# Kernel tuning notes

Hardware: AMD Instinct MI355X
Metric: run time of the kernel (lower is better)

Reference implementation:

```python
import jax, jax.numpy as jnp
import numpy as np
from math import factorial

P = 3          # polynomial order
D_I = 4096     # sketch output dim per order
C = 512        # input channels
B, H, W = 8, 28, 28
GAMMA = 1e-4


def setup_inputs() -> dict:
    key = jax.random.key(0)
    k1, k2, k3 = jax.random.split(key, 3)
    x = jax.random.normal(k1, (B, H, W, C), dtype=jnp.float32)
    # AlphaInitializer: alpha_i = sqrt(exp(-2g) * (2g)^i / i!)
    gam2 = np.full(P + 1, 2.0 * GAMMA)
    numer = np.power(gam2, np.arange(P + 1))
    denom = np.array([factorial(i) for i in range(P + 1)], dtype=np.float64)
    alpha = jnp.asarray(np.sqrt(np.exp(-gam2) * numer / denom), dtype=jnp.float32)
    # count-sketch hash indices and sign bits, one pair per order t in [0, p)
    h_idx = jax.random.randint(k2, (P, C), 0, D_I)
    s_bits = jax.random.randint(k3, (P, C), 0, 2).astype(jnp.int32)
    return {"x": x, "alpha": alpha, "h_idx": h_idx, "s_bits": s_bits}


def reference(x, alpha, h_idx, s_bits):
    Bs, Hs, Ws, Ch = x.shape
    p = h_idx.shape[0]
    d_i = D_I
    signs = (2 * s_bits - 1).astype(x.dtype)          # (p, C) in {-1,+1}
    x_flat = x.reshape(-1, Ch)                        # (B*H*W, C)

    def count_sketch(h, s):
        # scatter-add channels into d_i buckets: equivalent to x_flat @ S
        return jnp.zeros((x_flat.shape[0], d_i), x.dtype).at[:, h].add(x_flat * s)

    sk = jax.vmap(count_sketch)(h_idx, signs)         # (p, N, d_i)
    xs = jnp.transpose(sk, (1, 0, 2)).reshape(Bs, Hs * Ws, p, d_i)

    xf = jnp.fft.fft(xs.astype(jnp.complex64), axis=-1)
    cp = jnp.cumprod(xf, axis=-2)[:, :, 1:, :]        # orders 2..p
    xi = jnp.real(jnp.fft.ifft(cp, axis=-1)).mean(axis=1)   # (B, p-1, d_i)

    x_p = xi * alpha[2:].reshape(1, p - 1, 1)
    zeroth = alpha[0] * jnp.ones((Bs, 1), x.dtype)
    first = alpha[1] * x.mean(axis=(1, 2))            # (B, C)
    phi = jnp.concatenate([zeroth, first, x_p.reshape(Bs, -1)], axis=-1)
    phi = jnp.sign(phi) * jnp.sqrt(jnp.abs(phi) + 1e-12)    # signed sqrt
    return phi / jnp.linalg.norm(phi, axis=-1, keepdims=True)
```

## Files before the change

### kernel.cpp

```cpp
#include <hip/hip_runtime.h>

#define BATCH 8
#define NPOS 784
#define CH 512
#define DI 4096
#define PPC 8
#define CHUNKS (NPOS / PPC)
#define PHI_LEN 8705
#define REP 16
#define S_STRIDE (BATCH * 2 * 2049 * 2)
#define S_FLOATS (REP * S_STRIDE)
#define FO_OFF S_FLOATS
#define FO_STRIDE (BATCH * CH)
#define FO_FLOATS (REP * FO_STRIDE)
#define PH_OFF (FO_OFF + FO_FLOATS)
#define ZERO_FLOATS (S_FLOATS + FO_FLOATS)

__device__ __forceinline__ float2 cmul(float2 a, float2 b) {
  return make_float2(a.x * b.x - a.y * b.y, a.x * b.y + a.y * b.x);
}
__device__ __forceinline__ float2 f2add(float2 a, float2 b) {
  return make_float2(a.x + b.x, a.y + b.y);
}
__device__ __forceinline__ float2 f2sub(float2 a, float2 b) {
  return make_float2(a.x - b.x, a.y - b.y);
}

__device__ __forceinline__ void dft4(float2& a, float2& b, float2& c, float2& d) {
  float t0x = a.x + c.x, t0y = a.y + c.y;
  float t1x = a.x - c.x, t1y = a.y - c.y;
  float t2x = b.x + d.x, t2y = b.y + d.y;
  float t3x = b.x - d.x, t3y = b.y - d.y;
  a = make_float2(t0x + t2x, t0y + t2y);
  c = make_float2(t0x - t2x, t0y - t2y);
  b = make_float2(t1x + t3y, t1y - t3x);
  d = make_float2(t1x - t3y, t1y + t3x);
}

__device__ __forceinline__ void dft8(float2 v[8]) {
  float2 e0 = v[0], e1 = v[2], e2 = v[4], e3 = v[6];
  dft4(e0, e1, e2, e3);
  float2 o0 = v[1], o1 = v[3], o2 = v[5], o3 = v[7];
  dft4(o0, o1, o2, o3);
  const float r = 0.70710678118654752f;
  o1 = make_float2(r * (o1.x + o1.y), r * (o1.y - o1.x));
  o2 = make_float2(o2.y, -o2.x);
  o3 = make_float2(r * (o3.y - o3.x), -r * (o3.x + o3.y));
  v[0] = f2add(e0, o0); v[4] = f2sub(e0, o0);
  v[1] = f2add(e1, o1); v[5] = f2sub(e1, o1);
  v[2] = f2add(e2, o2); v[6] = f2sub(e2, o2);
  v[3] = f2add(e3, o3); v[7] = f2sub(e3, o3);
}

__device__ __forceinline__ void twiddle8(float2 v[8], float2 w) {
  float2 w2 = cmul(w, w);
  float2 w3 = cmul(w2, w);
  float2 w4 = cmul(w2, w2);
  v[1] = cmul(v[1], w);
  v[2] = cmul(v[2], w2);
  v[3] = cmul(v[3], w3);
  v[4] = cmul(v[4], w4);
  v[5] = cmul(v[5], cmul(w4, w));
  v[6] = cmul(v[6], cmul(w4, w2));
  v[7] = cmul(v[7], cmul(w4, w3));
}

__device__ __forceinline__ void s0w(float2* Z, int b) {
  const int base = b << 3;
  const int m0 = (b >> 1) & 15;
  float2 v[8];
  #pragma unroll
  for (int u = 0; u < 8; ++u) v[u] = Z[(base + u) ^ m0];
  dft8(v);
  #pragma unroll
  for (int k = 0; k < 8; ++k) Z[(base + k) ^ m0] = v[k];
}
__device__ __forceinline__ void s1w(float2* Z, int b, float2 w) {
  const int base = ((b >> 3) << 6) + (b & 7);
  const int g4 = (b >> 3) << 2;
  float2 v[8];
  #pragma unroll
  for (int u = 0; u < 8; ++u)
    v[u] = Z[(base + (u << 3)) ^ ((g4 + (u >> 1)) & 15)];
  twiddle8(v, w);
  dft8(v);
  #pragma unroll
  for (int k = 0; k < 8; ++k)
    Z[(base + (k << 3)) ^ ((g4 + (k >> 1)) & 15)] = v[k];
}
__device__ __forceinline__ void s2w(float2* Z, int b, float2 w) {
  const int base = ((b >> 6) << 9) + (b & 63);
  const int jh = (b & 63) >> 4;
  float2 v[8];
  #pragma unroll
  for (int u = 0; u < 8; ++u)
    v[u] = Z[(base + (u << 6)) ^ (((u << 2) + jh) & 15)];
  twiddle8(v, w);
  dft8(v);
  #pragma unroll
  for (int k = 0; k < 8; ++k)
    Z[(base + (k << 6)) ^ (((k << 2) + jh) & 15)] = v[k];
}
__device__ __forceinline__ void s3w(float2* Z, int b, float2 w) {
  const int m3 = (b >> 4) & 15;
  float2 v[8];
  #pragma unroll
  for (int u = 0; u < 8; ++u) v[u] = Z[(b + (u << 9)) ^ m3];
  twiddle8(v, w);
  dft8(v);
  #pragma unroll
  for (int k = 0; k < 8; ++k) Z[(b + (k << 9)) ^ m3] = v[k];
}

template <int MODE>
__device__ __forceinline__ void prodpair(float2 Zk, float2 Zm, float2& carry,
                                         float2& acc2, float2& acc3) {
  float2 E = make_float2(0.5f * (Zk.x + Zm.x), 0.5f * (Zk.y - Zm.y));
  float2 O = make_float2(0.5f * (Zk.y + Zm.y), -0.5f * (Zk.x - Zm.x));
  if (MODE == 0) {
    float2 P = cmul(E, O);
    carry = P;
    acc2.x += P.x; acc2.y += P.y;
  } else if (MODE == 1) {
    float2 P3 = cmul(carry, E);
    acc3.x += P3.x; acc3.y += P3.y;
    carry = O;
  } else {
    float2 P = cmul(carry, E);
    acc2.x += P.x; acc2.y += P.y;
    float2 P3 = cmul(P, O);
    acc3.x += P3.x; acc3.y += P3.y;
  }
}
template <int MODE>
__device__ __forceinline__ void nyq(float2 Zq, float& carryx, float& acc2x,
                                    float& acc3x) {
  if (MODE == 0) { carryx = Zq.x * Zq.y; acc2x += carryx; }
  else if (MODE == 1) { acc3x += carryx * Zq.x; carryx = Zq.y; }
  else { float tt = carryx * Zq.x; acc2x += tt; acc3x += tt * Zq.y; }
}

template <int MODE>
__device__ __forceinline__ void product_phase(float2* Z, int t,
                                              float2 carry[8], float2 acc2[8],
                                              float2 acc3[8], float& carryx,
                                              float& acc2x, float& acc3x) {
  const int mask3 = (t >> 4) & 15;
  #pragma unroll
  for (int jj = 0; jj < 8; ++jj) {
    const int k = t + (jj << 8);
    const int ak = k ^ mask3;
    const int m = (DI - k) & (DI - 1);
    const int am = m ^ ((m >> 4) & 15);
    float2 Zk = Z[ak], Zm = Z[am];
    Z[ak] = make_float2(0.f, 0.f);
    Z[am] = make_float2(0.f, 0.f);
    prodpair<MODE>(Zk, Zm, carry[jj], acc2[jj], acc3[jj]);
  }
  if (t == 0) {
    float2 Zq = Z[2048];
    Z[2048] = make_float2(0.f, 0.f);
    nyq<MODE>(Zq, carryx, acc2x, acc3x);
  }
}

__global__ __launch_bounds__(256) void cbp_stage1(
    const float* __restrict__ x, const float* __restrict__ alpha,
    const int* __restrict__ h_idx, const int* __restrict__ s_bits,
    float* __restrict__ ws) {
  __shared__ float2 Z[DI];
  float* Zf = (float*)Z;
  const int t = threadIdx.x;
  const int bb = blockIdx.x / CHUNKS;
  const int ch = blockIdx.x % CHUNKS;
  const int rep = blockIdx.x & (REP - 1);

  auto mapq = [](int h, int s) {
    int r = ((h & 7) << 9) | (((h >> 3) & 7) << 6) | (((h >> 6) & 7) << 3) |
            (h >> 9);
    return (r ^ ((r >> 4) & 15)) | ((s ^ 1) << 12);
  };
  auto sgn = [](float v, int q) {
    return __int_as_float(__float_as_int(v) ^ ((q & 0x1000) << 19));
  };
  const int c0 = t * 2, c1 = c0 + 1;
  const int qp0 = mapq(h_idx[c0], s_bits[c0]) |
                  (mapq(h_idx[c1], s_bits[c1]) << 13);
  const int qp1 = mapq(h_idx[CH + c0], s_bits[CH + c0]) |
                  (mapq(h_idx[CH + c1], s_bits[CH + c1]) << 13);
  const int qp2 = mapq(h_idx[2 * CH + c0], s_bits[2 * CH + c0]) |
                  (mapq(h_idx[2 * CH + c1], s_bits[2 * CH + c1]) << 13);

  float sv_, cv_;
  __sincosf(-9.8174770424681038e-2f * (float)(t & 7), &sv_, &cv_);
  const float2 w1b = make_float2(cv_, sv_);
  __sincosf(-1.2271846303085130e-2f * (float)(t & 63), &sv_, &cv_);
  const float2 w2b = make_float2(cv_, sv_);
  __sincosf(-1.5339807878856412e-3f * (float)t, &sv_, &cv_);
  const float2 w3b = make_float2(cv_, sv_);
  const float2 W256 = make_float2(0.92387953251128674f, -0.38268343236508977f);

  float2 acc2[8], acc3[8], carry[8];
  #pragma unroll
  for (int j = 0; j < 8; ++j) {
    acc2[j] = make_float2(0.f, 0.f);
    acc3[j] = make_float2(0.f, 0.f);
  }
  float acc2x = 0.f, acc3x = 0.f, carryx = 0.f;
  float xsa = 0.f, xsb = 0.f;

  #pragma unroll
  for (int q = 0; q < 16; ++q) Z[t + (q << 8)] = make_float2(0.f, 0.f);
  __syncthreads();

  #pragma unroll 1
  for (int ip = 0; ip < PPC / 2; ++ip) {
    const int n0 = bb * NPOS + ch * PPC + ip * 2;
    const float2 xv0 = *(const float2*)(x + (size_t)n0 * CH + c0);
    const float2 xv1 = *(const float2*)(x + (size_t)(n0 + 1) * CH + c0);
    xsa += xv0.x + xv1.x;
    xsb += xv0.y + xv1.y;

    #pragma unroll 1
    for (int f = 0; f < 3; ++f) {
      {
        const int qpr = (f == 0) ? qp0 : (f == 1) ? qp2 : qp1;
        const int qpi = (f == 0) ? qp1 : (f == 1) ? qp0 : qp2;
        const float vr0 = (f == 2) ? xv1.x : xv0.x;
        const float vr1 = (f == 2) ? xv1.y : xv0.y;
        const float vi0 = (f == 0) ? xv0.x : xv1.x;
        const float vi1 = (f == 0) ? xv0.y : xv1.y;
        const int qa = qpr & 0x1FFF, qb = (qpr >> 13) & 0x1FFF;
        const int ra = qpi & 0x1FFF, rb = (qpi >> 13) & 0x1FFF;
        atomicAdd(&Zf[2 * (qa & 0xFFF)], sgn(vr0, qa));
        atomicAdd(&Zf[2 * (qb & 0xFFF)], sgn(vr1, qb));
        atomicAdd(&Zf[2 * (ra & 0xFFF) + 1], sgn(vi0, ra));
        atomicAdd(&Zf[2 * (rb & 0xFFF) + 1], sgn(vi1, rb));
      }
      __syncthreads();
      #pragma unroll 1
      for (int h = 0; h < 2; ++h) s0w(Z, t + (h << 8));
      __builtin_amdgcn_wave_barrier();
      #pragma unroll 1
      for (int h = 0; h < 2; ++h) s1w(Z, t + (h << 8), w1b);
      __builtin_amdgcn_wave_barrier();
      #pragma unroll 1
      for (int h = 0; h < 2; ++h) s2w(Z, t + (h << 8), w2b);
      __syncthreads();
      #pragma unroll 1
      for (int h = 0; h < 2; ++h)
        s3w(Z, t + (h << 8), h ? cmul(w3b, W256) : w3b);
      __syncthreads();
      if (f == 0)
        product_phase<0>(Z, t, carry, acc2, acc3, carryx, acc2x, acc3x);
      else if (f == 1)
        product_phase<1>(Z, t, carry, acc2, acc3, carryx, acc2x, acc3x);
      else
        product_phase<2>(Z, t, carry, acc2, acc3, carryx, acc2x, acc3x);
      __syncthreads();
    }
  }

  float* S = ws + (size_t)rep * S_STRIDE;
  #pragma unroll
  for (int jj = 0; jj < 8; ++jj) {
    const int k = t + (jj << 8);
    float* p2p = S + ((size_t)(bb * 2 + 0) * 2049 + k) * 2;
    atomicAdd(p2p, acc2[jj].x);
    atomicAdd(p2p + 1, acc2[jj].y);
    float* p3p = S + ((size_t)(bb * 2 + 1) * 2049 + k) * 2;
    atomicAdd(p3p, acc3[jj].x);
    atomicAdd(p3p + 1, acc3[jj].y);
  }
  if (t == 0) {
    atomicAdd(S + ((size_t)(bb * 2 + 0) * 2049 + 2048) * 2, acc2x);
    atomicAdd(S + ((size_t)(bb * 2 + 1) * 2049 + 2048) * 2, acc3x);
  }

  const float sc1 = alpha[1] * (1.0f / (float)NPOS);
  atomicAdd(&ws[FO_OFF + (size_t)rep * FO_STRIDE + bb * CH + c0], xsa * sc1);
  atomicAdd(&ws[FO_OFF + (size_t)rep * FO_STRIDE + bb * CH + c1], xsb * sc1);
}

__device__ inline void fft4096_r2(float2* Z, const float2* W, int tid) {
  for (int s = 1; s <= 12; ++s) {
    __syncthreads();
    const int half = 1 << (s - 1);
    const int tsh = 12 - s;
    #pragma unroll
    for (int q = 0; q < 8; ++q) {
      int bidx = tid + q * 256;
      int j = bidx & (half - 1);
      int i1 = ((bidx >> (s - 1)) << s) + j;
      int i2 = i1 + half;
      float2 w = W[j << tsh];
      float2 u = Z[i1];
      float2 v = Z[i2];
      float2 t = cmul(w, v);
      Z[i1] = make_float2(u.x + t.x, u.y + t.y);
      Z[i2] = make_float2(u.x - t.x, u.y - t.y);
    }
  }
  __syncthreads();
}

__global__ __launch_bounds__(256) void cbp_stage2(
    const float* __restrict__ ws_in, const float* __restrict__ alpha,
    float* __restrict__ ws_out) {
  __shared__ float2 Z[DI];
  __shared__ float2 W[DI / 2];
  const int tid = threadIdx.x;

  for (int r = tid; r < DI / 2; r += 256) {
    float ang = 1.5339807878856412e-3f * (float)r;
    float sv, cv;
    sincosf(ang, &sv, &cv);
    W[r] = make_float2(cv, sv);
  }

  const int b = blockIdx.x >> 1;
  const int t = blockIdx.x & 1;
  const float* Sp = ws_in + ((size_t)(b * 2 + t) * 2049) * 2;

  for (int k = tid; k <= 2048; k += 256) {
    float re = 0.f, im = 0.f;
    #pragma unroll
    for (int rp = 0; rp < REP; ++rp) {
      re += Sp[(size_t)rp * S_STRIDE + k * 2];
      im += Sp[(size_t)rp * S_STRIDE + k * 2 + 1];
    }
    Z[__brev((unsigned)k) >> 20] = make_float2(re, im);
    if (k > 0 && k < 2048) {
      Z[__brev((unsigned)(DI - k)) >> 20] = make_float2(re, -im);
    }
  }
  fft4096_r2(Z, W, tid);

  const float scale = alpha[2 + t] / ((float)DI * (float)NPOS);
  float* out = ws_out + PH_OFF + (size_t)(b * 2 + t) * DI;
  for (int d = tid; d < DI; d += 256) out[d] = Z[d].x * scale;
}

__global__ __launch_bounds__(256) void cbp_stage3(
    const float* __restrict__ ws_in, const float* __restrict__ alpha,
    float* __restrict__ out) {
  __shared__ float red[4];
  const int b = blockIdx.x;
  const int tid = threadIdx.x;
  const float a0 = alpha[0];

  float w[35];
  float ssum = 0.f;
  #pragma unroll
  for (int j = 0; j < 35; ++j) {
    const int idx = tid + j * 256;
    float wv = 0.f;
    if (idx < PHI_LEN) {
      float v;
      if (idx == 0) {
        v = a0;
      } else if (idx <= 512) {
        v = 0.f;
        #pragma unroll
        for (int rp = 0; rp < REP; ++rp)
          v += ws_in[FO_OFF + (size_t)rp * FO_STRIDE + b * CH + (idx - 1)];
      } else {
        v = ws_in[PH_OFF + (size_t)b * 2 * DI + (idx - 513)];
      }
      float sq = sqrtf(fabsf(v) + 1e-12f);
      wv = (v > 0.f) ? sq : ((v < 0.f) ? -sq : 0.f);
    }
    w[j] = wv;
    ssum += wv * wv;
  }
  for (int off = 32; off > 0; off >>= 1) ssum += __shfl_down(ssum, off);
  if ((tid & 63) == 0) red[tid >> 6] = ssum;
  __syncthreads();
  const float tot = red[0] + red[1] + red[2] + red[3];
  const float inv = 1.0f / sqrtf(tot);

  #pragma unroll
  for (int j = 0; j < 35; ++j) {
    const int idx = tid + j * 256;
    if (idx < PHI_LEN) out[(size_t)b * PHI_LEN + idx] = w[j] * inv;
  }
}

extern "C" void kernel_launch(void* const* d_in, const int* in_sizes, int n_in,
                              void* d_out, int out_size, void* d_ws,
                              size_t ws_size, hipStream_t stream) {
  const float* x = (const float*)d_in[0];
  const float* alpha = (const float*)d_in[1];
  const int* h_idx = (const int*)d_in[2];
  const int* s_bits = (const int*)d_in[3];
  float* out = (float*)d_out;
  float* ws = (float*)d_ws;

  hipMemsetAsync(d_ws, 0, (size_t)ZERO_FLOATS * sizeof(float), stream);

  cbp_stage1<<<dim3(BATCH * CHUNKS), dim3(256), 0, stream>>>(x, alpha, h_idx,
                                                             s_bits, ws);
  cbp_stage2<<<dim3(BATCH * 2), dim3(256), 0, stream>>>(ws, alpha, ws);
  cbp_stage3<<<dim3(BATCH), dim3(256), 0, stream>>>(ws, alpha, out);
}
```

Measured before the change: 223.8 us.

## Interleave two FFT butterflies per thread and halve positions per block

Each FFT stage now has every thread load both of its radix-8 butterflies before computing, replacing the rolled two-iteration loop. Issuing the LDS loads together gives more memory-level parallelism and removes loop overhead. The s3 twiddle for the second half is precomputed once per thread. PPC is halved from 8 to 4, which doubles the number of blocks so the GPU has more parallelism, but also doubles the zeroing work and the final atomic accumulations. Keeping both butterflies live raises register pressure, which may reduce occupancy.

```diff
diff --git a/kernel.cpp b/kernel.cpp
--- a/kernel.cpp
+++ b/kernel.cpp
@@ -4,7 +4,7 @@
 #define NPOS 784
 #define CH 512
 #define DI 4096
-#define PPC 8
+#define PPC 4
 #define CHUNKS (NPOS / PPC)
 #define PHI_LEN 8705
 #define REP 16
@@ -65,51 +65,78 @@
   v[7] = cmul(v[7], cmul(w4, w3));
 }
 
-__device__ __forceinline__ void s0w(float2* Z, int b) {
-  const int base = b << 3;
-  const int m0 = (b >> 1) & 15;
-  float2 v[8];
-  #pragma unroll
-  for (int u = 0; u < 8; ++u) v[u] = Z[(base + u) ^ m0];
+__device__ __forceinline__ void s0w2(float2* Z, int t) {
+  const int base = t << 3;
+  const int m0 = (t >> 1) & 15;
+  float2 v[8], u[8];
+  #pragma unroll
+  for (int i = 0; i < 8; ++i) v[i] = Z[(base + i) ^ m0];
+  #pragma unroll
+  for (int i = 0; i < 8; ++i) u[i] = Z[(2048 + base + i) ^ m0];
   dft8(v);
   #pragma unroll
   for (int k = 0; k < 8; ++k) Z[(base + k) ^ m0] = v[k];
-}
-__device__ __forceinline__ void s1w(float2* Z, int b, float2 w) {
-  const int base = ((b >> 3) << 6) + (b & 7);
-  const int g4 = (b >> 3) << 2;
-  float2 v[8];
-  #pragma unroll
-  for (int u = 0; u < 8; ++u)
-    v[u] = Z[(base + (u << 3)) ^ ((g4 + (u >> 1)) & 15)];
+  dft8(u);
+  #pragma unroll
+  for (int k = 0; k < 8; ++k) Z[(2048 + base + k) ^ m0] = u[k];
+}
+__device__ __forceinline__ void s1w2(float2* Z, int t, float2 w) {
+  const int base = ((t >> 3) << 6) + (t & 7);
+  const int g4 = (t >> 3) << 2;
+  float2 v[8], u[8];
+  #pragma unroll
+  for (int i = 0; i < 8; ++i)
+    v[i] = Z[(base + (i << 3)) ^ ((g4 + (i >> 1)) & 15)];
+  #pragma unroll
+  for (int i = 0; i < 8; ++i)
+    u[i] = Z[(2048 + base + (i << 3)) ^ ((g4 + (i >> 1)) & 15)];
   twiddle8(v, w);
   dft8(v);
   #pragma unroll
   for (int k = 0; k < 8; ++k)
     Z[(base + (k << 3)) ^ ((g4 + (k >> 1)) & 15)] = v[k];
-}
-__device__ __forceinline__ void s2w(float2* Z, int b, float2 w) {
-  const int base = ((b >> 6) << 9) + (b & 63);
-  const int jh = (b & 63) >> 4;
-  float2 v[8];
-  #pragma unroll
-  for (int u = 0; u < 8; ++u)
-    v[u] = Z[(base + (u << 6)) ^ (((u << 2) + jh) & 15)];
+  twiddle8(u, w);
+  dft8(u);
+  #pragma unroll
+  for (int k = 0; k < 8; ++k)
+    Z[(2048 + base + (k << 3)) ^ ((g4 + (k >> 1)) & 15)] = u[k];
+}
+__device__ __forceinline__ void s2w2(float2* Z, int t, float2 w) {
+  const int base = ((t >> 6) << 9) + (t & 63);
+  const int jh = (t & 63) >> 4;
+  float2 v[8], u[8];
+  #pragma unroll
+  for (int i = 0; i < 8; ++i)
+    v[i] = Z[(base + (i << 6)) ^ (((i << 2) + jh) & 15)];
+  #pragma unroll
+  for (int i = 0; i < 8; ++i)
+    u[i] = Z[(2048 + base + (i << 6)) ^ (((i << 2) + jh) & 15)];
   twiddle8(v, w);
   dft8(v);
   #pragma unroll
   for (int k = 0; k < 8; ++k)
     Z[(base + (k << 6)) ^ (((k << 2) + jh) & 15)] = v[k];
-}
-__device__ __forceinline__ void s3w(float2* Z, int b, float2 w) {
-  const int m3 = (b >> 4) & 15;
-  float2 v[8];
-  #pragma unroll
-  for (int u = 0; u < 8; ++u) v[u] = Z[(b + (u << 9)) ^ m3];
-  twiddle8(v, w);
+  twiddle8(u, w);
+  dft8(u);
+  #pragma unroll
+  for (int k = 0; k < 8; ++k)
+    Z[(2048 + base + (k << 6)) ^ (((k << 2) + jh) & 15)] = u[k];
+}
+__device__ __forceinline__ void s3w2(float2* Z, int t, float2 wA, float2 wB) {
+  const int m3 = (t >> 4) & 15;
+  float2 v[8], u[8];
+  #pragma unroll
+  for (int i = 0; i < 8; ++i) v[i] = Z[(t + (i << 9)) ^ m3];
+  #pragma unroll
+  for (int i = 0; i < 8; ++i) u[i] = Z[(t + 256 + (i << 9)) ^ m3];
+  twiddle8(v, wA);
   dft8(v);
   #pragma unroll
-  for (int k = 0; k < 8; ++k) Z[(b + (k << 9)) ^ m3] = v[k];
+  for (int k = 0; k < 8; ++k) Z[(t + (k << 9)) ^ m3] = v[k];
+  twiddle8(u, wB);
+  dft8(u);
+  #pragma unroll
+  for (int k = 0; k < 8; ++k) Z[(t + 256 + (k << 9)) ^ m3] = u[k];
 }
 
 template <int MODE>
@@ -198,7 +225,8 @@
   const float2 w2b = make_float2(cv_, sv_);
   __sincosf(-1.5339807878856412e-3f * (float)t, &sv_, &cv_);
   const float2 w3b = make_float2(cv_, sv_);
-  const float2 W256 = make_float2(0.92387953251128674f, -0.38268343236508977f);
+  const float2 w3c = cmul(
+      w3b, make_float2(0.92387953251128674f, -0.38268343236508977f));
 
   float2 acc2[8], acc3[8], carry[8];
   #pragma unroll
@@ -238,18 +266,13 @@
         atomicAdd(&Zf[2 * (rb & 0xFFF) + 1], sgn(vi1, rb));
       }
       __syncthreads();
-      #pragma unroll 1
-      for (int h = 0; h < 2; ++h) s0w(Z, t + (h << 8));
+      s0w2(Z, t);
       __builtin_amdgcn_wave_barrier();
-      #pragma unroll 1
-      for (int h = 0; h < 2; ++h) s1w(Z, t + (h << 8), w1b);
+      s1w2(Z, t, w1b);
       __builtin_amdgcn_wave_barrier();
-      #pragma unroll 1
-      for (int h = 0; h < 2; ++h) s2w(Z, t + (h << 8), w2b);
+      s2w2(Z, t, w2b);
       __syncthreads();
-      #pragma unroll 1
-      for (int h = 0; h < 2; ++h)
-        s3w(Z, t + (h << 8), h ? cmul(w3b, W256) : w3b);
+      s3w2(Z, t, w3b, w3c);
       __syncthreads();
       if (f == 0)
         product_phase<0>(Z, t, carry, acc2, acc3, carryx, acc2x, acc3x);
```

Measured after the change: 269.7 us. 20.5% more time.
